# Kernel tuning notes

Measured on AMD Instinct MI355X. Metric: run time of the kernel, lower is better.

## Reference

```python
import jax, jax.numpy as jnp
import numpy as np

SHIFTS = [1, 2, 4]  # matches init_kwargs 'shifts' (all in range 0 < s < channels)


def setup_inputs() -> dict:
    key = jax.random.key(0)
    k1, k2, k3 = jax.random.split(key, 3)
    B, H, L, D = 4, 1, 2048, 512
    factor = 4
    proj_in = 2 * len(SHIFTS) * D  # cli_mode='full' -> 2 components per shift
    x = jax.random.normal(k1, (B, H, L, D), dtype=jnp.float32)
    W = jax.random.normal(k2, (factor, D), dtype=jnp.float32) * 0.05
    # glorot-ish scale for the projection kernel
    proj_kernel = jax.random.normal(k3, (proj_in, D), dtype=jnp.float32) * (1.0 / np.sqrt(proj_in))
    proj_bias = jnp.zeros((D,), dtype=jnp.float32)
    return {"x": x, "W": W, "proj_kernel": proj_kernel, "proj_bias": proj_bias}


def reference(x, W, proj_kernel, proj_bias):
    # x: (B, H, L, D); W: (k, D) slot multivectors
    k, D = W.shape
    B, H, L, _ = x.shape
    # coarse[-1] treated as zeros; non-anchor slots source previous coarse vector
    coarse_prev = jnp.pad(x, ((0, 0), (0, 0), (1, 0), (0, 0)))[:, :, :-1, :]
    # src: (B, H, L, k, D) — slots 0..k-2 from coarse_prev, slot k-1 (anchor) from x
    src = jnp.concatenate(
        [jnp.repeat(coarse_prev[:, :, :, None, :], k - 1, axis=3),
         x[:, :, :, None, :]],
        axis=3,
    )
    W_b = W[None, None, None, :, :]  # (1,1,1,k,D)
    components = []
    for s in SHIFTS:
        src_s = jnp.roll(src, s, axis=-1)
        W_s_b = jnp.roll(W, s, axis=-1)[None, None, None, :, :]
        sw = src * W_s_b
        components.append(sw - W_b * src_s)        # wedge part
        components.append(jax.nn.silu(sw))          # inner part (full mode)
    g = jnp.concatenate(components, axis=-1)  # (B,H,L,k, 2*len(shifts)*D)
    fine = jnp.einsum('bhlkc,cd->bhlkd', g, proj_kernel) + proj_bias
    return fine.reshape(B, H, L * k, D)
```

## Files before the change

kernel.cpp:

```cpp
#include <hip/hip_runtime.h>
#include <cstdint>
#include <cstddef>

#define D_DIM 512
#define L_DIM 2048
#define KB_DIM 2048
#define KS_DIM 1536
#define NROWS_X 2049
#define M_TOT 32768

typedef __bf16 bf16x8 __attribute__((ext_vector_type(8)));
typedef float  f32x4  __attribute__((ext_vector_type(4)));

__device__ __forceinline__ unsigned f2bf(float f) {
  unsigned u = __float_as_uint(f);
  u += 0x7FFF + ((u >> 16) & 1);
  return u >> 16;
}
__device__ __forceinline__ float bf2f(unsigned short u) {
  return __uint_as_float(((unsigned)u) << 16);
}
__device__ __forceinline__ void gld_lds16(const void* g, void* l) {
  __builtin_amdgcn_global_load_lds((const __attribute__((address_space(1))) void*)g,
                                   (__attribute__((address_space(3))) void*)l,
                                   16, 0, 0);
}

__global__ __launch_bounds__(256) void prep(
    const float* __restrict__ x, const float* __restrict__ W, const float* __restrict__ P,
    unsigned short* __restrict__ XbfZ, unsigned short* __restrict__ Ball,
    unsigned short* __restrict__ GS, int doGS) {
  __shared__ unsigned short WtabL[6144];
  const int tid = threadIdx.x;

  if (blockIdx.x < 2048) {
    for (int i = tid; i < 6144; i += 256) {
      const int c = i & 511; const int rest = i >> 9;
      const int si = rest % 3; const int jj = rest / 3;
      WtabL[i] = (unsigned short)f2bf(W[jj * 512 + ((c - (1 << si)) & 511)]);
    }
    __syncthreads();

    const int r = tid >> 6, lane = tid & 63;
    const int gr = blockIdx.x * 4 + r;
    const int b = gr >> 11, l = gr & 2047;

    const float4* xr = reinterpret_cast<const float4*>(x) + ((size_t)(b * L_DIM + l)) * 128 + lane * 2;
    const float4 v0 = xr[0], v1 = xr[1];
    union U { uint4 q; unsigned short s[8]; };
    U va;
    va.q.x = f2bf(v0.x) | (f2bf(v0.y) << 16);
    va.q.y = f2bf(v0.z) | (f2bf(v0.w) << 16);
    va.q.z = f2bf(v1.x) | (f2bf(v1.y) << 16);
    va.q.w = f2bf(v1.z) | (f2bf(v1.w) << 16);
    *reinterpret_cast<uint4*>(XbfZ + ((size_t)(b * NROWS_X + l + 1)) * 512 + lane * 8) = va.q;

    if (doGS) {
      #pragma unroll
      for (int j = 0; j < 4; ++j) {
        const int lam = (j < 3) ? (l + 1) : l;
        const bool wr = (j == 3) || (l < 2047);
        unsigned short* o = GS + ((size_t)((j * 4 + b) * L_DIM + lam)) * KS_DIM + lane * 8;
        #pragma unroll
        for (int si = 0; si < 3; ++si) {
          U wa;
          wa.q = *reinterpret_cast<const uint4*>(&WtabL[(j * 3 + si) * 512 + lane * 8]);
          unsigned res[4];
          #pragma unroll
          for (int e = 0; e < 4; ++e) {
            float s0 = bf2f(va.s[2 * e])     * bf2f(wa.s[2 * e]);
            float s1 = bf2f(va.s[2 * e + 1]) * bf2f(wa.s[2 * e + 1]);
            float g0 = s0 * __builtin_amdgcn_rcpf(1.f + __expf(-s0));
            float g1 = s1 * __builtin_amdgcn_rcpf(1.f + __expf(-s1));
            res[e] = f2bf(g0) | (f2bf(g1) << 16);
          }
          if (wr) {
            uint4 ov = {res[0], res[1], res[2], res[3]};
            *reinterpret_cast<uint4*>(o + si * 512) = ov;
          }
        }
      }
    }
    if (l == 2047) {
      const uint4 z = {0u, 0u, 0u, 0u};
      *reinterpret_cast<uint4*>(XbfZ + ((size_t)(b * NROWS_X)) * 512 + lane * 8) = z;
      if (doGS) {
        #pragma unroll
        for (int j = 0; j < 3; ++j)
          #pragma unroll
          for (int si = 0; si < 3; ++si)
            *reinterpret_cast<uint4*>(GS + ((size_t)((j * 4 + b) * L_DIM)) * KS_DIM + si * 512 + lane * 8) = z;
      }
    }
    return;
  }

  const int bx = blockIdx.x - 2048;
  const int j = bx >> 6, dt = (bx >> 3) & 7, ct = bx & 7;
  const int d = dt * 64 + (tid & 63);
  const int cbase = ct * 64 + (tid >> 6) * 16;
  unsigned short bufd[16];
  unsigned short bufs[3][16];
  #pragma unroll
  for (int cc = 0; cc < 16; ++cc) {
    const int c = cbase + cc;
    float qd = 0.f;
    #pragma unroll
    for (int si = 0; si < 3; ++si) {
      const int s = 1 << si;
      const int cm = (c - s) & 511, cp = (c + s) & 511;
      qd += W[j * 512 + cm] * P[((size_t)(2 * si) * 512 + c) * 512 + d]
          - W[j * 512 + cp] * P[((size_t)(2 * si) * 512 + cp) * 512 + d];
      bufs[si][cc] = (unsigned short)f2bf(P[((size_t)(2 * si + 1) * 512 + c) * 512 + d]);
    }
    bufd[cc] = (unsigned short)f2bf(qd);
  }
  unsigned short* row = Ball + (size_t)(j * 512 + d) * KB_DIM;
  *reinterpret_cast<uint4*>(&row[cbase])     = *reinterpret_cast<uint4*>(&bufd[0]);
  *reinterpret_cast<uint4*>(&row[cbase + 8]) = *reinterpret_cast<uint4*>(&bufd[8]);
  #pragma unroll
  for (int si = 0; si < 3; ++si) {
    *reinterpret_cast<uint4*>(&row[512 + si * 512 + cbase])     = *reinterpret_cast<uint4*>(&bufs[si][0]);
    *reinterpret_cast<uint4*>(&row[512 + si * 512 + cbase + 8]) = *reinterpret_cast<uint4*>(&bufs[si][8]);
  }
}

#define BARR asm volatile("s_barrier" ::: "memory")
#define VMW(N) asm volatile("s_waitcnt vmcnt(" #N ")" ::: "memory")

#define READ_A(MH, BUF) do { \
  _Pragma("unroll") \
  for (int mf = 0; mf < 4; ++mf) { \
    a[mf][0] = __builtin_bit_cast(bf16x8, *reinterpret_cast<const uint4*>(&A_lds[BUF][aRow[mf] + (MH)*4096 + p0])); \
    a[mf][1] = __builtin_bit_cast(bf16x8, *reinterpret_cast<const uint4*>(&A_lds[BUF][aRow[mf] + (MH)*4096 + p1])); \
  } } while (0)

#define READ_B(NH, BUF, BB) do { \
  _Pragma("unroll") \
  for (int nf = 0; nf < 2; ++nf) { \
    BB[nf][0] = __builtin_bit_cast(bf16x8, *reinterpret_cast<const uint4*>(&B_lds[BUF][bRow[nf] + (NH)*2048 + p0])); \
    BB[nf][1] = __builtin_bit_cast(bf16x8, *reinterpret_cast<const uint4*>(&B_lds[BUF][bRow[nf] + (NH)*2048 + p1])); \
  } } while (0)

#define MFMA_Q(MH, NH, BB) do { \
  _Pragma("unroll") \
  for (int mf = 0; mf < 4; ++mf) { \
    _Pragma("unroll") \
    for (int nf = 0; nf < 2; ++nf) { \
      acc[(MH)*4+mf][(NH)*2+nf] = __builtin_amdgcn_mfma_f32_16x16x32_bf16(a[mf][0], BB[nf][0], acc[(MH)*4+mf][(NH)*2+nf], 0, 0, 0); \
      acc[(MH)*4+mf][(NH)*2+nf] = __builtin_amdgcn_mfma_f32_16x16x32_bf16(a[mf][1], BB[nf][1], acc[(MH)*4+mf][(NH)*2+nf], 0, 0, 0); \
    } } } while (0)

__global__ __launch_bounds__(512, 2) void gemm8(
    const unsigned short* __restrict__ XbfZ, const unsigned short* __restrict__ GS,
    const unsigned short* __restrict__ Ball, const float* __restrict__ bias,
    float* __restrict__ out) {
  __shared__ alignas(16) unsigned short A_lds[2][16384];
  __shared__ alignas(16) unsigned short B_lds[2][16384];

  const int tid = threadIdx.x;
  const int bid = blockIdx.x;
  const int wid = (bid & 7) * 32 + (bid >> 3);
  const int mtile = wid >> 1;
  const int ntile = wid & 1;
  const int j  = mtile >> 5;
  const int b  = (mtile >> 3) & 3;
  const int l0 = (mtile & 7) * 256;
  const int n0 = ntile * 256;
  const size_t mbase = (size_t)((j * 4 + b) * L_DIM + l0);

  const int srow = tid >> 3;
  const int c8   = (tid & 7) ^ (srow & 7);
  const unsigned short* pXd = XbfZ + ((size_t)(b * NROWS_X + (j == 3) + l0 + srow)) * 512 + c8 * 8;
  const unsigned short* pGS = GS + (mbase + srow) * (size_t)KS_DIM + c8 * 8;
  const unsigned short* pB  = Ball + ((size_t)(j * 512 + n0 + srow)) * KB_DIM + c8 * 8;
  const int ldsSlot = tid * 8;

  auto stageA = [&](int TT, int h, int bufi) {
    unsigned short* dst = &A_lds[bufi][h * 8192 + ldsSlot];
    if (TT < 8) {
      const unsigned short* s = pXd + (size_t)h * 128 * 512 + TT * 64;
      gld_lds16(s, dst);
      gld_lds16(s + 64 * 512, dst + 4096);
    } else {
      const unsigned short* s = pGS + (size_t)h * 128 * KS_DIM + (TT - 8) * 64;
      gld_lds16(s, dst);
      gld_lds16(s + 64 * KS_DIM, dst + 4096);
    }
  };
  auto stageB = [&](int TT, int h, int bufi) {
    const unsigned short* s = pB + (size_t)h * 128 * KB_DIM + TT * 64;
    unsigned short* dst = &B_lds[bufi][h * 8192 + ldsSlot];
    gld_lds16(s, dst);
    gld_lds16(s + 64 * KB_DIM, dst + 4096);
  };

  const int lane = tid & 63, wv = tid >> 6;
  const int wm = wv >> 2, wn = wv & 3;
  const int l16 = lane & 15, quad = lane >> 4;
  const int p0 = ((quad)     ^ (l16 & 7)) * 8;
  const int p1 = ((quad + 4) ^ (l16 & 7)) * 8;
  int aRow[4], bRow[2];
  #pragma unroll
  for (int mf = 0; mf < 4; ++mf) aRow[mf] = (wm * 128 + mf * 16 + l16) * 64;
  #pragma unroll
  for (int nf = 0; nf < 2; ++nf) bRow[nf] = (wn * 64 + nf * 16 + l16) * 64;

  f32x4 acc[8][4];
  #pragma unroll
  for (int i = 0; i < 8; ++i)
    #pragma unroll
    for (int n = 0; n < 4; ++n)
      acc[i][n] = f32x4{0.f, 0.f, 0.f, 0.f};

  bf16x8 a[4][2], b0[2][2], b1[2][2];

  stageB(0, 0, 0); stageB(0, 1, 0);
  stageA(0, 0, 0); stageA(0, 1, 0);
  stageB(1, 0, 1); stageB(1, 1, 1);
  VMW(4);
  BARR;

  for (int T = 0; T < 32; ++T) {
    const int cur = T & 1, nxt = cur ^ 1;
    if (T + 1 < 32) { stageA(T + 1, 0, nxt); stageA(T + 1, 1, nxt); }
    READ_A(0, cur);
    READ_B(0, cur, b0);
    READ_B(1, cur, b1);
    __builtin_amdgcn_s_setprio(1);
    MFMA_Q(0, 0, b0);
    MFMA_Q(0, 1, b1);
    __builtin_amdgcn_s_setprio(0);
    BARR;
    if (T + 2 < 32) { stageB(T + 2, 0, cur); stageB(T + 2, 1, cur); }
    READ_A(1, cur);
    __builtin_amdgcn_s_setprio(1);
    MFMA_Q(1, 1, b1);
    MFMA_Q(1, 0, b0);
    __builtin_amdgcn_s_setprio(0);
    if (T < 30) {
      VMW(4);
      BARR;
    } else if (T == 30) {
      VMW(0);
      BARR;
    }
  }

  #pragma unroll
  for (int nfg = 0; nfg < 4; ++nfg) {
    const int d = n0 + wn * 64 + nfg * 16 + l16;
    const float bv = bias[d];
    #pragma unroll
    for (int mfg = 0; mfg < 8; ++mfg) {
      const int lrow = l0 + wm * 128 + mfg * 16 + quad * 4;
      #pragma unroll
      for (int rg = 0; rg < 4; ++rg) {
        out[((size_t)(b * L_DIM + lrow + rg) * 4 + j) * D_DIM + d] = acc[mfg][nfg][rg] + bv;
      }
    }
  }
}

__global__ __launch_bounds__(256, 2) void fused_gemm(
    const unsigned short* __restrict__ XbfZ, const unsigned short* __restrict__ Ball,
    const float* __restrict__ W, const float* __restrict__ bias,
    float* __restrict__ out) {
  __shared__ alignas(16) unsigned short Vt[2][4096];
  __shared__ alignas(16) unsigned short Bt[2][8192];
  __shared__ alignas(16) unsigned short At[128 * 40];
  __shared__ alignas(16) unsigned short Wr[3 * 512];

  const int tid = threadIdx.x;
  const int nt = blockIdx.x & 1;
  const int mt = blockIdx.x >> 1;
  const int j  = mt >> 6;
  const int b  = (mt >> 4) & 3;
  const int lt = mt & 15;
  const int l0 = lt * 128;
  const int n0 = nt * 256;
  const int base_l = l0 - ((j == 3) ? 0 : 1);

  #pragma unroll
  for (int i = 0; i < 6; ++i) {
    const int idx = tid + i * 256;
    const int si = idx >> 9, c = idx & 511, s = 1 << si;
    Wr[idx] = (unsigned short)f2bf(W[j * 512 + ((c - s) & 511)]);
  }

  const int lane = tid & 63, wv = tid >> 6;
  const int qv = (lane & 3) ^ ((lane >> 4) & 3);
  const int rsub = lane >> 2;
  const unsigned short* gA0 = XbfZ + ((size_t)(b * NROWS_X + 1 + base_l + (wv * 2) * 16 + rsub)) * 512 + qv * 8;
  const unsigned short* gA1 = gA0 + (size_t)16 * 512;
  const unsigned short* gB[4];
  #pragma unroll
  for (int pi = 0; pi < 4; ++pi)
    gB[pi] = Ball + (size_t)(j * 512 + n0 + (wv * 4 + pi) * 16 + rsub) * KB_DIM + qv * 8;
  const int vOff0 = wv * 1024 + lane * 8;
  const int bOff0 = wv * 2048 + lane * 8;

  const int am = tid >> 1;
  const int akh = (tid & 1) * 16;
  const int ch0 = (tid & 1) * 2;
  const int sswz = (am >> 2) & 3;
  unsigned short* aDst = &At[am * 40 + akh];

  const int l16 = lane & 15, quad = lane >> 4;
  const int wm = wv >> 1, wn = wv & 1;
  const int fsw = (l16 >> 2) & 3;
  const int aVoff = (wm * 64 + l16) * 32 + ((quad ^ fsw)) * 8;
  const int aSoff = (wm * 64 + l16) * 40 + quad * 8;
  const int bOffF = (wn * 128 + l16) * 32 + ((quad ^ fsw)) * 8;

  f32x4 acc[4][8];
  #pragma unroll
  for (int i = 0; i < 4; ++i)
    #pragma unroll
    for (int n = 0; n < 8; ++n)
      acc[i][n] = f32x4{0.f, 0.f, 0.f, 0.f};

  {
    gld_lds16(gA0, &Vt[0][vOff0]);
    gld_lds16(gA1, &Vt[0][vOff0 + 512]);
    #pragma unroll
    for (int pi = 0; pi < 4; ++pi)
      gld_lds16(gB[pi], &Bt[0][bOff0 + pi * 512]);
  }

  for (int it = 0; it < 64; ++it) {
    const int buf = it & 1;
    const int kk0 = it * 32;
    const int gi = kk0 >> 9;

    __syncthreads();

    if (it + 1 < 64) {
      const int nk = kk0 + 32;
      const int nv = nk & 511;
      gld_lds16(gA0 + nv, &Vt[buf ^ 1][vOff0]);
      gld_lds16(gA1 + nv, &Vt[buf ^ 1][vOff0 + 512]);
      #pragma unroll
      for (int pi = 0; pi < 4; ++pi)
        gld_lds16(gB[pi] + nk, &Bt[buf ^ 1][bOff0 + pi * 512]);
    }

    bf16x8 af[4], bfr[8];
    if (gi == 0) {
      #pragma unroll
      for (int mi = 0; mi < 4; ++mi) {
        uint4 r = *reinterpret_cast<const uint4*>(&Vt[buf][aVoff + mi * 512]);
        af[mi] = __builtin_bit_cast(bf16x8, r);
      }
    } else {
      const int si = gi - 1;
      const int ccbase = (kk0 & 511) + akh;
      uint4 v0 = *reinterpret_cast<const uint4*>(&Vt[buf][(am * 4 + ((ch0)     ^ sswz)) * 8]);
      uint4 v1 = *reinterpret_cast<const uint4*>(&Vt[buf][(am * 4 + ((ch0 + 1) ^ sswz)) * 8]);
      uint4 w0 = *reinterpret_cast<const uint4*>(&Wr[si * 512 + ccbase]);
      uint4 w1 = *reinterpret_cast<const uint4*>(&Wr[si * 512 + ccbase + 8]);
      union U { uint4 q[2]; unsigned short s[16]; };
      U va, wa; va.q[0] = v0; va.q[1] = v1; wa.q[0] = w0; wa.q[1] = w1;
      unsigned res[8];
      #pragma unroll
      for (int e = 0; e < 8; ++e) {
        float s0 = bf2f(va.s[2 * e])     * bf2f(wa.s[2 * e]);
        float s1 = bf2f(va.s[2 * e + 1]) * bf2f(wa.s[2 * e + 1]);
        float g0 = s0 * __builtin_amdgcn_rcpf(1.f + __expf(-s0));
        float g1 = s1 * __builtin_amdgcn_rcpf(1.f + __expf(-s1));
        res[e] = f2bf(g0) | (f2bf(g1) << 16);
      }
      uint4 o0 = {res[0], res[1], res[2], res[3]};
      uint4 o1 = {res[4], res[5], res[6], res[7]};
      *reinterpret_cast<uint4*>(aDst) = o0;
      *reinterpret_cast<uint4*>(aDst + 8) = o1;
      __syncthreads();
      #pragma unroll
      for (int mi = 0; mi < 4; ++mi) {
        uint4 r = *reinterpret_cast<const uint4*>(&At[aSoff + mi * 640]);
        af[mi] = __builtin_bit_cast(bf16x8, r);
      }
    }
    #pragma unroll
    for (int ni = 0; ni < 8; ++ni) {
      uint4 r = *reinterpret_cast<const uint4*>(&Bt[buf][bOffF + ni * 512]);
      bfr[ni] = __builtin_bit_cast(bf16x8, r);
    }
    #pragma unroll
    for (int mi = 0; mi < 4; ++mi)
      #pragma unroll
      for (int ni = 0; ni < 8; ++ni)
        acc[mi][ni] = __builtin_amdgcn_mfma_f32_16x16x32_bf16(af[mi], bfr[ni], acc[mi][ni], 0, 0, 0);
  }

  #pragma unroll
  for (int ni = 0; ni < 8; ++ni) {
    const int d = n0 + wn * 128 + ni * 16 + l16;
    const float bv = bias[d];
    #pragma unroll
    for (int mi = 0; mi < 4; ++mi) {
      const int lrow = l0 + wm * 64 + mi * 16 + quad * 4;
      #pragma unroll
      for (int rg = 0; rg < 4; ++rg) {
        out[((size_t)(b * L_DIM + lrow + rg) * 4 + j) * D_DIM + d] = acc[mi][ni][rg] + bv;
      }
    }
  }
}

extern "C" void kernel_launch(void* const* d_in, const int* in_sizes, int n_in,
                              void* d_out, int out_size, void* d_ws, size_t ws_size,
                              hipStream_t stream) {
  const float* x    = (const float*)d_in[0];
  const float* W    = (const float*)d_in[1];
  const float* P    = (const float*)d_in[2];
  const float* bias = (const float*)d_in[3];
  float* out = (float*)d_out;

  unsigned short* XbfZ = (unsigned short*)d_ws;
  unsigned short* Ball = XbfZ + (size_t)4 * NROWS_X * 512;
  unsigned short* GS   = Ball + (size_t)4 * 512 * KB_DIM + 6144;
  const size_t need_bytes =
      ((size_t)4 * NROWS_X * 512 + (size_t)4 * 512 * KB_DIM + 6144 +
       (size_t)M_TOT * KS_DIM) * 2;
  const bool primary = ws_size >= need_bytes;

  prep<<<2304, 256, 0, stream>>>(x, W, P, XbfZ, Ball, GS, primary ? 1 : 0);
  if (primary) {
    gemm8<<<dim3(256), dim3(512), 0, stream>>>(XbfZ, GS, Ball, bias, out);
  } else {
    fused_gemm<<<512, 256, 0, stream>>>(XbfZ, Ball, W, bias, out);
  }
}
```

Measured before the change: 175.5 us.

## Compute SiLU operand on the fly inside GEMM instead of materializing GS buffer

The prep kernel no longer writes the large bf16 SiLU operand buffer (GS, about 100MB); it only converts x to bf16 and builds the folded weight matrix. The GEMM now computes the SiLU(x*W_shift) A-tiles itself. For each k-tile it reads the x row from global into registers, applies the product and SiLU after the first MFMA half, and writes the result into the swizzled LDS buffer. K-tiles are interleaved so each x chunk is reused across the three shifts. This removes a large write and re-read of global memory, at the cost of extra VALU work and register loads inside the GEMM pipeline, plus added lgkmcnt waits.

Result: slower. 189.2 us (+7.8%).

```diff
diff --git a/kernel.cpp b/kernel.cpp
--- a/kernel.cpp
+++ b/kernel.cpp
@@ -5,9 +5,7 @@
 #define D_DIM 512
 #define L_DIM 2048
 #define KB_DIM 2048
-#define KS_DIM 1536
 #define NROWS_X 2049
-#define M_TOT 32768
 
 typedef __bf16 bf16x8 __attribute__((ext_vector_type(8)));
 typedef float  f32x4  __attribute__((ext_vector_type(4)));
@@ -28,74 +26,27 @@
 
 __global__ __launch_bounds__(256) void prep(
     const float* __restrict__ x, const float* __restrict__ W, const float* __restrict__ P,
-    unsigned short* __restrict__ XbfZ, unsigned short* __restrict__ Ball,
-    unsigned short* __restrict__ GS, int doGS) {
-  __shared__ unsigned short WtabL[6144];
+    unsigned short* __restrict__ XbfZ, unsigned short* __restrict__ Ball) {
   const int tid = threadIdx.x;
-
-  if (blockIdx.x < 2048) {
-    for (int i = tid; i < 6144; i += 256) {
-      const int c = i & 511; const int rest = i >> 9;
-      const int si = rest % 3; const int jj = rest / 3;
-      WtabL[i] = (unsigned short)f2bf(W[jj * 512 + ((c - (1 << si)) & 511)]);
-    }
-    __syncthreads();
-
-    const int r = tid >> 6, lane = tid & 63;
-    const int gr = blockIdx.x * 4 + r;
-    const int b = gr >> 11, l = gr & 2047;
-
-    const float4* xr = reinterpret_cast<const float4*>(x) + ((size_t)(b * L_DIM + l)) * 128 + lane * 2;
-    const float4 v0 = xr[0], v1 = xr[1];
-    union U { uint4 q; unsigned short s[8]; };
-    U va;
-    va.q.x = f2bf(v0.x) | (f2bf(v0.y) << 16);
-    va.q.y = f2bf(v0.z) | (f2bf(v0.w) << 16);
-    va.q.z = f2bf(v1.x) | (f2bf(v1.y) << 16);
-    va.q.w = f2bf(v1.z) | (f2bf(v1.w) << 16);
-    *reinterpret_cast<uint4*>(XbfZ + ((size_t)(b * NROWS_X + l + 1)) * 512 + lane * 8) = va.q;
-
-    if (doGS) {
-      #pragma unroll
-      for (int j = 0; j < 4; ++j) {
-        const int lam = (j < 3) ? (l + 1) : l;
-        const bool wr = (j == 3) || (l < 2047);
-        unsigned short* o = GS + ((size_t)((j * 4 + b) * L_DIM + lam)) * KS_DIM + lane * 8;
-        #pragma unroll
-        for (int si = 0; si < 3; ++si) {
-          U wa;
-          wa.q = *reinterpret_cast<const uint4*>(&WtabL[(j * 3 + si) * 512 + lane * 8]);
-          unsigned res[4];
-          #pragma unroll
-          for (int e = 0; e < 4; ++e) {
-            float s0 = bf2f(va.s[2 * e])     * bf2f(wa.s[2 * e]);
-            float s1 = bf2f(va.s[2 * e + 1]) * bf2f(wa.s[2 * e + 1]);
-            float g0 = s0 * __builtin_amdgcn_rcpf(1.f + __expf(-s0));
-            float g1 = s1 * __builtin_amdgcn_rcpf(1.f + __expf(-s1));
-            res[e] = f2bf(g0) | (f2bf(g1) << 16);
-          }
-          if (wr) {
-            uint4 ov = {res[0], res[1], res[2], res[3]};
-            *reinterpret_cast<uint4*>(o + si * 512) = ov;
-          }
-        }
-      }
-    }
-    if (l == 2047) {
-      const uint4 z = {0u, 0u, 0u, 0u};
-      *reinterpret_cast<uint4*>(XbfZ + ((size_t)(b * NROWS_X)) * 512 + lane * 8) = z;
-      if (doGS) {
-        #pragma unroll
-        for (int j = 0; j < 3; ++j)
-          #pragma unroll
-          for (int si = 0; si < 3; ++si)
-            *reinterpret_cast<uint4*>(GS + ((size_t)((j * 4 + b) * L_DIM)) * KS_DIM + si * 512 + lane * 8) = z;
-      }
-    }
+  if (blockIdx.x >= 256) {
+    const int u = (blockIdx.x - 256) * 256 + tid;
+    const int b = u / (NROWS_X * 64);
+    const int rr = (u >> 6) % NROWS_X;
+    const int c8 = u & 63;
+    uint4 p = {0u, 0u, 0u, 0u};
+    if (rr > 0) {
+      const float4* src = reinterpret_cast<const float4*>(x) +
+                          ((size_t)(b * L_DIM + rr - 1)) * 128 + c8 * 2;
+      const float4 v0 = src[0], v1 = src[1];
+      p.x = f2bf(v0.x) | (f2bf(v0.y) << 16);
+      p.y = f2bf(v0.z) | (f2bf(v0.w) << 16);
+      p.z = f2bf(v1.x) | (f2bf(v1.y) << 16);
+      p.w = f2bf(v1.z) | (f2bf(v1.w) << 16);
+    }
+    reinterpret_cast<uint4*>(XbfZ)[((size_t)(b * NROWS_X + rr)) * 64 + c8] = p;
     return;
   }
-
-  const int bx = blockIdx.x - 2048;
+  const int bx = blockIdx.x;
   const int j = bx >> 6, dt = (bx >> 3) & 7, ct = bx & 7;
   const int d = dt * 64 + (tid & 63);
   const int cbase = ct * 64 + (tid >> 6) * 16;
@@ -127,6 +78,8 @@
 
 #define BARR asm volatile("s_barrier" ::: "memory")
 #define VMW(N) asm volatile("s_waitcnt vmcnt(" #N ")" ::: "memory")
+#define LGKM0 asm volatile("s_waitcnt lgkmcnt(0)" ::: "memory")
+#define KT(S) (((((S) & 3)) << 3) + ((S) >> 2))
 
 #define READ_A(MH, BUF) do { \
   _Pragma("unroll") \
@@ -151,12 +104,13 @@
       acc[(MH)*4+mf][(NH)*2+nf] = __builtin_amdgcn_mfma_f32_16x16x32_bf16(a[mf][1], BB[nf][1], acc[(MH)*4+mf][(NH)*2+nf], 0, 0, 0); \
     } } } while (0)
 
-__global__ __launch_bounds__(512, 2) void gemm8(
-    const unsigned short* __restrict__ XbfZ, const unsigned short* __restrict__ GS,
-    const unsigned short* __restrict__ Ball, const float* __restrict__ bias,
+__global__ __launch_bounds__(512, 2) void gemmcs(
+    const unsigned short* __restrict__ XbfZ, const unsigned short* __restrict__ Ball,
+    const float* __restrict__ W, const float* __restrict__ bias,
     float* __restrict__ out) {
   __shared__ alignas(16) unsigned short A_lds[2][16384];
   __shared__ alignas(16) unsigned short B_lds[2][16384];
+  __shared__ alignas(16) unsigned short Wt[1536];
 
   const int tid = threadIdx.x;
   const int bid = blockIdx.x;
@@ -167,33 +121,40 @@
   const int b  = (mtile >> 3) & 3;
   const int l0 = (mtile & 7) * 256;
   const int n0 = ntile * 256;
-  const size_t mbase = (size_t)((j * 4 + b) * L_DIM + l0);
+
+  for (int i = tid; i < 1536; i += 512) {
+    const int si = i >> 9, c = i & 511;
+    Wt[i] = (unsigned short)f2bf(W[j * 512 + ((c - (1 << si)) & 511)]);
+  }
 
   const int srow = tid >> 3;
   const int c8   = (tid & 7) ^ (srow & 7);
   const unsigned short* pXd = XbfZ + ((size_t)(b * NROWS_X + (j == 3) + l0 + srow)) * 512 + c8 * 8;
-  const unsigned short* pGS = GS + (mbase + srow) * (size_t)KS_DIM + c8 * 8;
   const unsigned short* pB  = Ball + ((size_t)(j * 512 + n0 + srow)) * KB_DIM + c8 * 8;
   const int ldsSlot = tid * 8;
 
-  auto stageA = [&](int TT, int h, int bufi) {
-    unsigned short* dst = &A_lds[bufi][h * 8192 + ldsSlot];
-    if (TT < 8) {
-      const unsigned short* s = pXd + (size_t)h * 128 * 512 + TT * 64;
+  auto stageXd = [&](int cb, int bufi) {
+    #pragma unroll
+    for (int h = 0; h < 2; ++h) {
+      const unsigned short* s = pXd + (size_t)h * 128 * 512 + cb * 64;
+      unsigned short* dst = &A_lds[bufi][h * 8192 + ldsSlot];
       gld_lds16(s, dst);
       gld_lds16(s + 64 * 512, dst + 4096);
-    } else {
-      const unsigned short* s = pGS + (size_t)h * 128 * KS_DIM + (TT - 8) * 64;
+    }
+  };
+  auto stageB = [&](int kt, int bufi) {
+    #pragma unroll
+    for (int h = 0; h < 2; ++h) {
+      const unsigned short* s = pB + (size_t)h * 128 * KB_DIM + kt * 64;
+      unsigned short* dst = &B_lds[bufi][h * 8192 + ldsSlot];
       gld_lds16(s, dst);
-      gld_lds16(s + 64 * KS_DIM, dst + 4096);
+      gld_lds16(s + 64 * KB_DIM, dst + 4096);
     }
   };
-  auto stageB = [&](int TT, int h, int bufi) {
-    const unsigned short* s = pB + (size_t)h * 128 * KB_DIM + TT * 64;
-    unsigned short* dst = &B_lds[bufi][h * 8192 + ldsSlot];
-    gld_lds16(s, dst);
-    gld_lds16(s + 64 * KB_DIM, dst + 4096);
-  };
+
+  const int prow = tid >> 1;
+  const int phalf = tid & 1;
+  const unsigned short* pXr = XbfZ + ((size_t)(b * NROWS_X + (j == 3) + l0 + prow)) * 512 + phalf * 32;
 
   const int lane = tid & 63, wv = tid >> 6;
   const int wm = wv >> 2, wn = wv & 3;
@@ -215,15 +176,27 @@
 
   bf16x8 a[4][2], b0[2][2], b1[2][2];
 
-  stageB(0, 0, 0); stageB(0, 1, 0);
-  stageA(0, 0, 0); stageA(0, 1, 0);
-  stageB(1, 0, 1); stageB(1, 1, 1);
+  stageXd(0, 0);
+  stageB(KT(0), 0);
+  stageB(KT(1), 1);
+  LGKM0;
   VMW(4);
   BARR;
 
-  for (int T = 0; T < 32; ++T) {
-    const int cur = T & 1, nxt = cur ^ 1;
-    if (T + 1 < 32) { stageA(T + 1, 0, nxt); stageA(T + 1, 1, nxt); }
+  for (int s = 0; s < 32; ++s) {
+    const int cur = s & 1, nxt = cur ^ 1;
+    const int f1 = (s + 1) & 3;
+    const int cb1 = (s + 1) >> 2;
+    uint4 xv[4];
+    if (s < 31) {
+      if (f1 == 0) {
+        stageXd(cb1, nxt);
+      } else {
+        #pragma unroll
+        for (int k = 0; k < 4; ++k)
+          xv[k] = *reinterpret_cast<const uint4*>(pXr + cb1 * 64 + k * 8);
+      }
+    }
     READ_A(0, cur);
     READ_B(0, cur, b0);
     READ_B(1, cur, b1);
@@ -232,16 +205,42 @@
     MFMA_Q(0, 1, b1);
     __builtin_amdgcn_s_setprio(0);
     BARR;
-    if (T + 2 < 32) { stageB(T + 2, 0, cur); stageB(T + 2, 1, cur); }
+    if (s < 31 && f1 != 0) {
+      VMW(0);
+      const int si = f1 - 1;
+      const int wtbase = si * 512 + cb1 * 64 + phalf * 32;
+      #pragma unroll
+      for (int k = 0; k < 4; ++k) {
+        union UU { uint4 q; unsigned short sh[8]; } vv, ww;
+        vv.q = xv[k];
+        ww.q = *reinterpret_cast<const uint4*>(&Wt[wtbase + k * 8]);
+        unsigned res[4];
+        #pragma unroll
+        for (int e = 0; e < 4; ++e) {
+          float s0 = bf2f(vv.sh[2 * e])     * bf2f(ww.sh[2 * e]);
+          float s1 = bf2f(vv.sh[2 * e + 1]) * bf2f(ww.sh[2 * e + 1]);
+          float g0 = s0 * __builtin_amdgcn_rcpf(1.f + __expf(-s0));
+          float g1 = s1 * __builtin_amdgcn_rcpf(1.f + __expf(-s1));
+          res[e] = f2bf(g0) | (f2bf(g1) << 16);
+        }
+        const int lc = phalf * 4 + k;
+        const int pos = lc ^ (prow & 7);
+        uint4 ov = {res[0], res[1], res[2], res[3]};
+        *reinterpret_cast<uint4*>(&A_lds[nxt][prow * 64 + pos * 8]) = ov;
+      }
+    }
+    if (s + 2 < 32) stageB(KT(s + 2), cur);
     READ_A(1, cur);
     __builtin_amdgcn_s_setprio(1);
     MFMA_Q(1, 1, b1);
     MFMA_Q(1, 0, b0);
     __builtin_amdgcn_s_setprio(0);
-    if (T < 30) {
+    if (s < 30) {
+      LGKM0;
       VMW(4);
       BARR;
-    } else if (T == 30) {
+    } else if (s == 30) {
+      LGKM0;
       VMW(0);
       BARR;
     }
@@ -257,152 +256,6 @@
       #pragma unroll
       for (int rg = 0; rg < 4; ++rg) {
         out[((size_t)(b * L_DIM + lrow + rg) * 4 + j) * D_DIM + d] = acc[mfg][nfg][rg] + bv;
-      }
-    }
-  }
-}
-
-__global__ __launch_bounds__(256, 2) void fused_gemm(
-    const unsigned short* __restrict__ XbfZ, const unsigned short* __restrict__ Ball,
-    const float* __restrict__ W, const float* __restrict__ bias,
-    float* __restrict__ out) {
-  __shared__ alignas(16) unsigned short Vt[2][4096];
-  __shared__ alignas(16) unsigned short Bt[2][8192];
-  __shared__ alignas(16) unsigned short At[128 * 40];
-  __shared__ alignas(16) unsigned short Wr[3 * 512];
-
-  const int tid = threadIdx.x;
-  const int nt = blockIdx.x & 1;
-  const int mt = blockIdx.x >> 1;
-  const int j  = mt >> 6;
-  const int b  = (mt >> 4) & 3;
-  const int lt = mt & 15;
-  const int l0 = lt * 128;
-  const int n0 = nt * 256;
-  const int base_l = l0 - ((j == 3) ? 0 : 1);
-
-  #pragma unroll
-  for (int i = 0; i < 6; ++i) {
-    const int idx = tid + i * 256;
-    const int si = idx >> 9, c = idx & 511, s = 1 << si;
-    Wr[idx] = (unsigned short)f2bf(W[j * 512 + ((c - s) & 511)]);
-  }
-
-  const int lane = tid & 63, wv = tid >> 6;
-  const int qv = (lane & 3) ^ ((lane >> 4) & 3);
-  const int rsub = lane >> 2;
-  const unsigned short* gA0 = XbfZ + ((size_t)(b * NROWS_X + 1 + base_l + (wv * 2) * 16 + rsub)) * 512 + qv * 8;
-  const unsigned short* gA1 = gA0 + (size_t)16 * 512;
-  const unsigned short* gB[4];
-  #pragma unroll
-  for (int pi = 0; pi < 4; ++pi)
-    gB[pi] = Ball + (size_t)(j * 512 + n0 + (wv * 4 + pi) * 16 + rsub) * KB_DIM + qv * 8;
-  const int vOff0 = wv * 1024 + lane * 8;
-  const int bOff0 = wv * 2048 + lane * 8;
-
-  const int am = tid >> 1;
-  const int akh = (tid & 1) * 16;
-  const int ch0 = (tid & 1) * 2;
-  const int sswz = (am >> 2) & 3;
-  unsigned short* aDst = &At[am * 40 + akh];
-
-  const int l16 = lane & 15, quad = lane >> 4;
-  const int wm = wv >> 1, wn = wv & 1;
-  const int fsw = (l16 >> 2) & 3;
-  const int aVoff = (wm * 64 + l16) * 32 + ((quad ^ fsw)) * 8;
-  const int aSoff = (wm * 64 + l16) * 40 + quad * 8;
-  const int bOffF = (wn * 128 + l16) * 32 + ((quad ^ fsw)) * 8;
-
-  f32x4 acc[4][8];
-  #pragma unroll
-  for (int i = 0; i < 4; ++i)
-    #pragma unroll
-    for (int n = 0; n < 8; ++n)
-      acc[i][n] = f32x4{0.f, 0.f, 0.f, 0.f};
-
-  {
-    gld_lds16(gA0, &Vt[0][vOff0]);
-    gld_lds16(gA1, &Vt[0][vOff0 + 512]);
-    #pragma unroll
-    for (int pi = 0; pi < 4; ++pi)
-      gld_lds16(gB[pi], &Bt[0][bOff0 + pi * 512]);
-  }
-
-  for (int it = 0; it < 64; ++it) {
-    const int buf = it & 1;
-    const int kk0 = it * 32;
-    const int gi = kk0 >> 9;
-
-    __syncthreads();
-
-    if (it + 1 < 64) {
-      const int nk = kk0 + 32;
-      const int nv = nk & 511;
-      gld_lds16(gA0 + nv, &Vt[buf ^ 1][vOff0]);
-      gld_lds16(gA1 + nv, &Vt[buf ^ 1][vOff0 + 512]);
-      #pragma unroll
-      for (int pi = 0; pi < 4; ++pi)
-        gld_lds16(gB[pi] + nk, &Bt[buf ^ 1][bOff0 + pi * 512]);
-    }
-
-    bf16x8 af[4], bfr[8];
-    if (gi == 0) {
-      #pragma unroll
-      for (int mi = 0; mi < 4; ++mi) {
-        uint4 r = *reinterpret_cast<const uint4*>(&Vt[buf][aVoff + mi * 512]);
-        af[mi] = __builtin_bit_cast(bf16x8, r);
-      }
-    } else {
-      const int si = gi - 1;
-      const int ccbase = (kk0 & 511) + akh;
-      uint4 v0 = *reinterpret_cast<const uint4*>(&Vt[buf][(am * 4 + ((ch0)     ^ sswz)) * 8]);
-      uint4 v1 = *reinterpret_cast<const uint4*>(&Vt[buf][(am * 4 + ((ch0 + 1) ^ sswz)) * 8]);
-      uint4 w0 = *reinterpret_cast<const uint4*>(&Wr[si * 512 + ccbase]);
-      uint4 w1 = *reinterpret_cast<const uint4*>(&Wr[si * 512 + ccbase + 8]);
-      union U { uint4 q[2]; unsigned short s[16]; };
-      U va, wa; va.q[0] = v0; va.q[1] = v1; wa.q[0] = w0; wa.q[1] = w1;
-      unsigned res[8];
-      #pragma unroll
-      for (int e = 0; e < 8; ++e) {
-        float s0 = bf2f(va.s[2 * e])     * bf2f(wa.s[2 * e]);
-        float s1 = bf2f(va.s[2 * e + 1]) * bf2f(wa.s[2 * e + 1]);
-        float g0 = s0 * __builtin_amdgcn_rcpf(1.f + __expf(-s0));
-        float g1 = s1 * __builtin_amdgcn_rcpf(1.f + __expf(-s1));
-        res[e] = f2bf(g0) | (f2bf(g1) << 16);
-      }
-      uint4 o0 = {res[0], res[1], res[2], res[3]};
-      uint4 o1 = {res[4], res[5], res[6], res[7]};
-      *reinterpret_cast<uint4*>(aDst) = o0;
-      *reinterpret_cast<uint4*>(aDst + 8) = o1;
-      __syncthreads();
-      #pragma unroll
-      for (int mi = 0; mi < 4; ++mi) {
-        uint4 r = *reinterpret_cast<const uint4*>(&At[aSoff + mi * 640]);
-        af[mi] = __builtin_bit_cast(bf16x8, r);
-      }
-    }
-    #pragma unroll
-    for (int ni = 0; ni < 8; ++ni) {
-      uint4 r = *reinterpret_cast<const uint4*>(&Bt[buf][bOffF + ni * 512]);
-      bfr[ni] = __builtin_bit_cast(bf16x8, r);
-    }
-    #pragma unroll
-    for (int mi = 0; mi < 4; ++mi)
-      #pragma unroll
-      for (int ni = 0; ni < 8; ++ni)
-        acc[mi][ni] = __builtin_amdgcn_mfma_f32_16x16x32_bf16(af[mi], bfr[ni], acc[mi][ni], 0, 0, 0);
-  }
-
-  #pragma unroll
-  for (int ni = 0; ni < 8; ++ni) {
-    const int d = n0 + wn * 128 + ni * 16 + l16;
-    const float bv = bias[d];
-    #pragma unroll
-    for (int mi = 0; mi < 4; ++mi) {
-      const int lrow = l0 + wm * 64 + mi * 16 + quad * 4;
-      #pragma unroll
-      for (int rg = 0; rg < 4; ++rg) {
-        out[((size_t)(b * L_DIM + lrow + rg) * 4 + j) * D_DIM + d] = acc[mi][ni][rg] + bv;
       }
     }
   }
@@ -419,16 +272,7 @@
 
   unsigned short* XbfZ = (unsigned short*)d_ws;
   unsigned short* Ball = XbfZ + (size_t)4 * NROWS_X * 512;
-  unsigned short* GS   = Ball + (size_t)4 * 512 * KB_DIM + 6144;
-  const size_t need_bytes =
-      ((size_t)4 * NROWS_X * 512 + (size_t)4 * 512 * KB_DIM + 6144 +
-       (size_t)M_TOT * KS_DIM) * 2;
-  const bool primary = ws_size >= need_bytes;
-
-  prep<<<2304, 256, 0, stream>>>(x, W, P, XbfZ, Ball, GS, primary ? 1 : 0);
-  if (primary) {
-    gemm8<<<dim3(256), dim3(512), 0, stream>>>(XbfZ, GS, Ball, bias, out);
-  } else {
-    fused_gemm<<<512, 256, 0, stream>>>(XbfZ, Ball, W, bias, out);
-  }
-}
+
+  prep<<<2305, 256, 0, stream>>>(x, W, P, XbfZ, Ball);
+  gemmcs<<<dim3(256), dim3(512), 0, stream>>>(XbfZ, Ball, W, bias, out);
+}
```

## Triple-buffer A tiles in LDS and reorder MFMA issue per k-chunk

Applied to the files above, without the earlier changes.

The A operand moves from double to triple buffering in LDS. Each A tile is now prefetched two k-steps ahead, matching B, and the wait count is raised so two stages stay in flight. The MFMA loop is reordered to walk k-chunks outermost and reuse each A fragment across all four N fragments. This is meant to hide more global-to-LDS latency behind the matrix work. In exchange it grows LDS per block to 160KB, which fills the CU's LDS and rules out a second resident block.

Result: no change. 175.8 us (+0.2%).

```diff
diff --git a/kernel.cpp b/kernel.cpp
--- a/kernel.cpp
+++ b/kernel.cpp
@@ -128,34 +128,36 @@
 #define BARR asm volatile("s_barrier" ::: "memory")
 #define VMW(N) asm volatile("s_waitcnt vmcnt(" #N ")" ::: "memory")
 
-#define READ_A(MH, BUF) do { \
+#define READ_A(MH, AP) do { \
   _Pragma("unroll") \
   for (int mf = 0; mf < 4; ++mf) { \
-    a[mf][0] = __builtin_bit_cast(bf16x8, *reinterpret_cast<const uint4*>(&A_lds[BUF][aRow[mf] + (MH)*4096 + p0])); \
-    a[mf][1] = __builtin_bit_cast(bf16x8, *reinterpret_cast<const uint4*>(&A_lds[BUF][aRow[mf] + (MH)*4096 + p1])); \
+    a[mf][0] = __builtin_bit_cast(bf16x8, *reinterpret_cast<const uint4*>(&(AP)[aRow[mf] + (MH)*4096 + p0])); \
+    a[mf][1] = __builtin_bit_cast(bf16x8, *reinterpret_cast<const uint4*>(&(AP)[aRow[mf] + (MH)*4096 + p1])); \
   } } while (0)
 
-#define READ_B(NH, BUF, BB) do { \
+#define READ_B(NH, BP, BB) do { \
   _Pragma("unroll") \
   for (int nf = 0; nf < 2; ++nf) { \
-    BB[nf][0] = __builtin_bit_cast(bf16x8, *reinterpret_cast<const uint4*>(&B_lds[BUF][bRow[nf] + (NH)*2048 + p0])); \
-    BB[nf][1] = __builtin_bit_cast(bf16x8, *reinterpret_cast<const uint4*>(&B_lds[BUF][bRow[nf] + (NH)*2048 + p1])); \
+    BB[nf][0] = __builtin_bit_cast(bf16x8, *reinterpret_cast<const uint4*>(&(BP)[bRow[nf] + (NH)*2048 + p0])); \
+    BB[nf][1] = __builtin_bit_cast(bf16x8, *reinterpret_cast<const uint4*>(&(BP)[bRow[nf] + (NH)*2048 + p1])); \
   } } while (0)
 
-#define MFMA_Q(MH, NH, BB) do { \
+#define MFMA_ROW(MH) do { \
   _Pragma("unroll") \
-  for (int mf = 0; mf < 4; ++mf) { \
+  for (int kc = 0; kc < 2; ++kc) { \
     _Pragma("unroll") \
-    for (int nf = 0; nf < 2; ++nf) { \
-      acc[(MH)*4+mf][(NH)*2+nf] = __builtin_amdgcn_mfma_f32_16x16x32_bf16(a[mf][0], BB[nf][0], acc[(MH)*4+mf][(NH)*2+nf], 0, 0, 0); \
-      acc[(MH)*4+mf][(NH)*2+nf] = __builtin_amdgcn_mfma_f32_16x16x32_bf16(a[mf][1], BB[nf][1], acc[(MH)*4+mf][(NH)*2+nf], 0, 0, 0); \
+    for (int mf = 0; mf < 4; ++mf) { \
+      acc[(MH)*4+mf][0] = __builtin_amdgcn_mfma_f32_16x16x32_bf16(a[mf][kc], b0[0][kc], acc[(MH)*4+mf][0], 0, 0, 0); \
+      acc[(MH)*4+mf][1] = __builtin_amdgcn_mfma_f32_16x16x32_bf16(a[mf][kc], b0[1][kc], acc[(MH)*4+mf][1], 0, 0, 0); \
+      acc[(MH)*4+mf][2] = __builtin_amdgcn_mfma_f32_16x16x32_bf16(a[mf][kc], b1[0][kc], acc[(MH)*4+mf][2], 0, 0, 0); \
+      acc[(MH)*4+mf][3] = __builtin_amdgcn_mfma_f32_16x16x32_bf16(a[mf][kc], b1[1][kc], acc[(MH)*4+mf][3], 0, 0, 0); \
     } } } while (0)
 
 __global__ __launch_bounds__(512, 2) void gemm8(
     const unsigned short* __restrict__ XbfZ, const unsigned short* __restrict__ GS,
     const unsigned short* __restrict__ Ball, const float* __restrict__ bias,
     float* __restrict__ out) {
-  __shared__ alignas(16) unsigned short A_lds[2][16384];
+  __shared__ alignas(16) unsigned short A_lds[3][16384];
   __shared__ alignas(16) unsigned short B_lds[2][16384];
 
   const int tid = threadIdx.x;
@@ -176,23 +178,29 @@
   const unsigned short* pB  = Ball + ((size_t)(j * 512 + n0 + srow)) * KB_DIM + c8 * 8;
   const int ldsSlot = tid * 8;
 
-  auto stageA = [&](int TT, int h, int bufi) {
-    unsigned short* dst = &A_lds[bufi][h * 8192 + ldsSlot];
-    if (TT < 8) {
-      const unsigned short* s = pXd + (size_t)h * 128 * 512 + TT * 64;
+  auto stageA = [&](int TT, int bufi) {
+    #pragma unroll
+    for (int h = 0; h < 2; ++h) {
+      unsigned short* dst = &A_lds[bufi][h * 8192 + ldsSlot];
+      if (TT < 8) {
+        const unsigned short* s = pXd + (size_t)h * 128 * 512 + TT * 64;
+        gld_lds16(s, dst);
+        gld_lds16(s + 64 * 512, dst + 4096);
+      } else {
+        const unsigned short* s = pGS + (size_t)h * 128 * KS_DIM + (TT - 8) * 64;
+        gld_lds16(s, dst);
+        gld_lds16(s + 64 * KS_DIM, dst + 4096);
+      }
+    }
+  };
+  auto stageB = [&](int TT, int bufi) {
+    #pragma unroll
+    for (int h = 0; h < 2; ++h) {
+      const unsigned short* s = pB + (size_t)h * 128 * KB_DIM + TT * 64;
+      unsigned short* dst = &B_lds[bufi][h * 8192 + ldsSlot];
       gld_lds16(s, dst);
-      gld_lds16(s + 64 * 512, dst + 4096);
-    } else {
-      const unsigned short* s = pGS + (size_t)h * 128 * KS_DIM + (TT - 8) * 64;
-      gld_lds16(s, dst);
-      gld_lds16(s + 64 * KS_DIM, dst + 4096);
-    }
-  };
-  auto stageB = [&](int TT, int h, int bufi) {
-    const unsigned short* s = pB + (size_t)h * 128 * KB_DIM + TT * 64;
-    unsigned short* dst = &B_lds[bufi][h * 8192 + ldsSlot];
-    gld_lds16(s, dst);
-    gld_lds16(s + 64 * KB_DIM, dst + 4096);
+      gld_lds16(s + 64 * KB_DIM, dst + 4096);
+    }
   };
 
   const int lane = tid & 63, wv = tid >> 6;
@@ -215,36 +223,40 @@
 
   bf16x8 a[4][2], b0[2][2], b1[2][2];
 
-  stageB(0, 0, 0); stageB(0, 1, 0);
-  stageA(0, 0, 0); stageA(0, 1, 0);
-  stageB(1, 0, 1); stageB(1, 1, 1);
-  VMW(4);
+  stageA(0, 0);
+  stageB(0, 0);
+  stageA(1, 1);
+  stageB(1, 1);
+  VMW(8);
   BARR;
 
+  int ra = 0;
   for (int T = 0; T < 32; ++T) {
-    const int cur = T & 1, nxt = cur ^ 1;
-    if (T + 1 < 32) { stageA(T + 1, 0, nxt); stageA(T + 1, 1, nxt); }
-    READ_A(0, cur);
-    READ_B(0, cur, b0);
-    READ_B(1, cur, b1);
+    const int cur = T & 1;
+    const int rs = (ra >= 1) ? (ra - 1) : 2;
+    const unsigned short* Ac = A_lds[ra];
+    const unsigned short* Bc = B_lds[cur];
+    if (T + 2 < 32) stageA(T + 2, rs);
+    READ_A(0, Ac);
+    READ_B(0, Bc, b0);
+    READ_B(1, Bc, b1);
     __builtin_amdgcn_s_setprio(1);
-    MFMA_Q(0, 0, b0);
-    MFMA_Q(0, 1, b1);
+    MFMA_ROW(0);
     __builtin_amdgcn_s_setprio(0);
     BARR;
-    if (T + 2 < 32) { stageB(T + 2, 0, cur); stageB(T + 2, 1, cur); }
-    READ_A(1, cur);
+    if (T + 2 < 32) stageB(T + 2, cur);
+    READ_A(1, Ac);
     __builtin_amdgcn_s_setprio(1);
-    MFMA_Q(1, 1, b1);
-    MFMA_Q(1, 0, b0);
+    MFMA_ROW(1);
     __builtin_amdgcn_s_setprio(0);
     if (T < 30) {
-      VMW(4);
+      VMW(8);
       BARR;
     } else if (T == 30) {
       VMW(0);
       BARR;
     }
+    ra = (ra >= 2) ? 0 : (ra + 1);
   }
 
   #pragma unroll
```

## Replace 256x256 GEMM tiles with 128x128 tiles and a triple-buffered K pipeline

Applied to the files above, without the earlier changes.

The primary GEMM moves from 256 blocks of 512 threads on 256x256 tiles (K step 64, double buffered) to 1024 blocks of 256 threads on 128x128 tiles (K step 32, three LDS stages, prefetch distance 2). The LDS swizzle and fragment offsets are rebuilt for the 32-wide rows. The aim is more blocks per CU and better latency hiding on a 256-CU part. The cost is less operand reuse per tile, more global and LDS traffic, and twice as many barriers along K.

Result: slower. 206.7 us (+17.7%).

```diff
diff --git a/kernel.cpp b/kernel.cpp
--- a/kernel.cpp
+++ b/kernel.cpp
@@ -128,135 +128,114 @@
 #define BARR asm volatile("s_barrier" ::: "memory")
 #define VMW(N) asm volatile("s_waitcnt vmcnt(" #N ")" ::: "memory")
 
-#define READ_A(MH, BUF) do { \
-  _Pragma("unroll") \
-  for (int mf = 0; mf < 4; ++mf) { \
-    a[mf][0] = __builtin_bit_cast(bf16x8, *reinterpret_cast<const uint4*>(&A_lds[BUF][aRow[mf] + (MH)*4096 + p0])); \
-    a[mf][1] = __builtin_bit_cast(bf16x8, *reinterpret_cast<const uint4*>(&A_lds[BUF][aRow[mf] + (MH)*4096 + p1])); \
-  } } while (0)
-
-#define READ_B(NH, BUF, BB) do { \
-  _Pragma("unroll") \
-  for (int nf = 0; nf < 2; ++nf) { \
-    BB[nf][0] = __builtin_bit_cast(bf16x8, *reinterpret_cast<const uint4*>(&B_lds[BUF][bRow[nf] + (NH)*2048 + p0])); \
-    BB[nf][1] = __builtin_bit_cast(bf16x8, *reinterpret_cast<const uint4*>(&B_lds[BUF][bRow[nf] + (NH)*2048 + p1])); \
-  } } while (0)
-
-#define MFMA_Q(MH, NH, BB) do { \
-  _Pragma("unroll") \
-  for (int mf = 0; mf < 4; ++mf) { \
-    _Pragma("unroll") \
-    for (int nf = 0; nf < 2; ++nf) { \
-      acc[(MH)*4+mf][(NH)*2+nf] = __builtin_amdgcn_mfma_f32_16x16x32_bf16(a[mf][0], BB[nf][0], acc[(MH)*4+mf][(NH)*2+nf], 0, 0, 0); \
-      acc[(MH)*4+mf][(NH)*2+nf] = __builtin_amdgcn_mfma_f32_16x16x32_bf16(a[mf][1], BB[nf][1], acc[(MH)*4+mf][(NH)*2+nf], 0, 0, 0); \
-    } } } while (0)
-
-__global__ __launch_bounds__(512, 2) void gemm8(
+__global__ __launch_bounds__(256, 3) void gemm128(
     const unsigned short* __restrict__ XbfZ, const unsigned short* __restrict__ GS,
     const unsigned short* __restrict__ Ball, const float* __restrict__ bias,
     float* __restrict__ out) {
-  __shared__ alignas(16) unsigned short A_lds[2][16384];
-  __shared__ alignas(16) unsigned short B_lds[2][16384];
+  __shared__ alignas(16) unsigned short A_lds[3][4096];
+  __shared__ alignas(16) unsigned short B_lds[3][4096];
 
   const int tid = threadIdx.x;
   const int bid = blockIdx.x;
-  const int wid = (bid & 7) * 32 + (bid >> 3);
-  const int mtile = wid >> 1;
-  const int ntile = wid & 1;
-  const int j  = mtile >> 5;
-  const int b  = (mtile >> 3) & 3;
-  const int l0 = (mtile & 7) * 256;
-  const int n0 = ntile * 256;
+  const int wid = (bid & 7) * 128 + (bid >> 3);
+  const int mtile = wid >> 2;
+  const int ntile = wid & 3;
+  const int j  = mtile >> 6;
+  const int b  = (mtile >> 4) & 3;
+  const int l0 = (mtile & 15) * 128;
+  const int n0 = ntile * 128;
   const size_t mbase = (size_t)((j * 4 + b) * L_DIM + l0);
 
-  const int srow = tid >> 3;
-  const int c8   = (tid & 7) ^ (srow & 7);
-  const unsigned short* pXd = XbfZ + ((size_t)(b * NROWS_X + (j == 3) + l0 + srow)) * 512 + c8 * 8;
-  const unsigned short* pGS = GS + (mbase + srow) * (size_t)KS_DIM + c8 * 8;
-  const unsigned short* pB  = Ball + ((size_t)(j * 512 + n0 + srow)) * KB_DIM + c8 * 8;
+  const int srow = tid >> 2;
+  const int spos = tid & 3;
+  const int sc   = spos ^ (srow & 3) ^ ((srow >> 2) & 3);
+  const unsigned short* pXd = XbfZ + ((size_t)(b * NROWS_X + (j == 3) + l0 + srow)) * 512 + sc * 8;
+  const unsigned short* pGS = GS + (mbase + srow) * (size_t)KS_DIM + sc * 8;
+  const unsigned short* pB  = Ball + ((size_t)(j * 512 + n0 + srow)) * KB_DIM + sc * 8;
   const int ldsSlot = tid * 8;
 
-  auto stageA = [&](int TT, int h, int bufi) {
-    unsigned short* dst = &A_lds[bufi][h * 8192 + ldsSlot];
-    if (TT < 8) {
-      const unsigned short* s = pXd + (size_t)h * 128 * 512 + TT * 64;
+  auto stageA = [&](int TT, int bufi) {
+    unsigned short* dst = &A_lds[bufi][ldsSlot];
+    if (TT < 16) {
+      const unsigned short* s = pXd + TT * 32;
       gld_lds16(s, dst);
-      gld_lds16(s + 64 * 512, dst + 4096);
+      gld_lds16(s + 64 * 512, dst + 2048);
     } else {
-      const unsigned short* s = pGS + (size_t)h * 128 * KS_DIM + (TT - 8) * 64;
+      const unsigned short* s = pGS + (TT - 16) * 32;
       gld_lds16(s, dst);
-      gld_lds16(s + 64 * KS_DIM, dst + 4096);
+      gld_lds16(s + 64 * KS_DIM, dst + 2048);
     }
   };
-  auto stageB = [&](int TT, int h, int bufi) {
-    const unsigned short* s = pB + (size_t)h * 128 * KB_DIM + TT * 64;
-    unsigned short* dst = &B_lds[bufi][h * 8192 + ldsSlot];
+  auto stageB = [&](int TT, int bufi) {
+    const unsigned short* s = pB + TT * 32;
+    unsigned short* dst = &B_lds[bufi][ldsSlot];
     gld_lds16(s, dst);
-    gld_lds16(s + 64 * KB_DIM, dst + 4096);
+    gld_lds16(s + 64 * KB_DIM, dst + 2048);
   };
 
   const int lane = tid & 63, wv = tid >> 6;
-  const int wm = wv >> 2, wn = wv & 3;
+  const int wm = wv >> 1, wn = wv & 1;
   const int l16 = lane & 15, quad = lane >> 4;
-  const int p0 = ((quad)     ^ (l16 & 7)) * 8;
-  const int p1 = ((quad + 4) ^ (l16 & 7)) * 8;
-  int aRow[4], bRow[2];
-  #pragma unroll
-  for (int mf = 0; mf < 4; ++mf) aRow[mf] = (wm * 128 + mf * 16 + l16) * 64;
-  #pragma unroll
-  for (int nf = 0; nf < 2; ++nf) bRow[nf] = (wn * 64 + nf * 16 + l16) * 64;
-
-  f32x4 acc[8][4];
-  #pragma unroll
-  for (int i = 0; i < 8; ++i)
+  const int rp = (quad ^ (l16 & 3) ^ ((l16 >> 2) & 3)) * 8;
+  int aOff[4], bOff[4];
+  #pragma unroll
+  for (int mf = 0; mf < 4; ++mf) aOff[mf] = (wm * 64 + mf * 16 + l16) * 32 + rp;
+  #pragma unroll
+  for (int nf = 0; nf < 4; ++nf) bOff[nf] = (wn * 64 + nf * 16 + l16) * 32 + rp;
+
+  f32x4 acc[4][4];
+  #pragma unroll
+  for (int i = 0; i < 4; ++i)
     #pragma unroll
     for (int n = 0; n < 4; ++n)
       acc[i][n] = f32x4{0.f, 0.f, 0.f, 0.f};
 
-  bf16x8 a[4][2], b0[2][2], b1[2][2];
-
-  stageB(0, 0, 0); stageB(0, 1, 0);
-  stageA(0, 0, 0); stageA(0, 1, 0);
-  stageB(1, 0, 1); stageB(1, 1, 1);
+  bf16x8 a[4], bf[4];
+
+  stageA(0, 0); stageB(0, 0);
+  stageA(1, 1); stageB(1, 1);
   VMW(4);
   BARR;
 
-  for (int T = 0; T < 32; ++T) {
-    const int cur = T & 1, nxt = cur ^ 1;
-    if (T + 1 < 32) { stageA(T + 1, 0, nxt); stageA(T + 1, 1, nxt); }
-    READ_A(0, cur);
-    READ_B(0, cur, b0);
-    READ_B(1, cur, b1);
+  int cur = 0;
+  for (int T = 0; T < 64; ++T) {
+    const int rs = (cur >= 1) ? (cur - 1) : 2;
+    if (T + 2 < 64) { stageA(T + 2, rs); stageB(T + 2, rs); }
+    const unsigned short* Ac = A_lds[cur];
+    const unsigned short* Bc = B_lds[cur];
+    #pragma unroll
+    for (int mf = 0; mf < 4; ++mf)
+      a[mf] = __builtin_bit_cast(bf16x8, *reinterpret_cast<const uint4*>(&Ac[aOff[mf]]));
+    #pragma unroll
+    for (int nf = 0; nf < 4; ++nf)
+      bf[nf] = __builtin_bit_cast(bf16x8, *reinterpret_cast<const uint4*>(&Bc[bOff[nf]]));
     __builtin_amdgcn_s_setprio(1);
-    MFMA_Q(0, 0, b0);
-    MFMA_Q(0, 1, b1);
+    #pragma unroll
+    for (int mf = 0; mf < 4; ++mf)
+      #pragma unroll
+      for (int nf = 0; nf < 4; ++nf)
+        acc[mf][nf] = __builtin_amdgcn_mfma_f32_16x16x32_bf16(a[mf], bf[nf], acc[mf][nf], 0, 0, 0);
     __builtin_amdgcn_s_setprio(0);
-    BARR;
-    if (T + 2 < 32) { stageB(T + 2, 0, cur); stageB(T + 2, 1, cur); }
-    READ_A(1, cur);
-    __builtin_amdgcn_s_setprio(1);
-    MFMA_Q(1, 1, b1);
-    MFMA_Q(1, 0, b0);
-    __builtin_amdgcn_s_setprio(0);
-    if (T < 30) {
+    if (T < 62) {
       VMW(4);
       BARR;
-    } else if (T == 30) {
+    } else if (T == 62) {
       VMW(0);
       BARR;
     }
-  }
-
-  #pragma unroll
-  for (int nfg = 0; nfg < 4; ++nfg) {
-    const int d = n0 + wn * 64 + nfg * 16 + l16;
+    cur = (cur >= 2) ? 0 : (cur + 1);
+  }
+
+  #pragma unroll
+  for (int nf = 0; nf < 4; ++nf) {
+    const int d = n0 + wn * 64 + nf * 16 + l16;
     const float bv = bias[d];
     #pragma unroll
-    for (int mfg = 0; mfg < 8; ++mfg) {
-      const int lrow = l0 + wm * 128 + mfg * 16 + quad * 4;
+    for (int mf = 0; mf < 4; ++mf) {
+      const int lrow = l0 + wm * 64 + mf * 16 + quad * 4;
       #pragma unroll
       for (int rg = 0; rg < 4; ++rg) {
-        out[((size_t)(b * L_DIM + lrow + rg) * 4 + j) * D_DIM + d] = acc[mfg][nfg][rg] + bv;
+        out[((size_t)(b * L_DIM + lrow + rg) * 4 + j) * D_DIM + d] = acc[mf][nf][rg] + bv;
       }
     }
   }
@@ -427,7 +406,7 @@
 
   prep<<<2304, 256, 0, stream>>>(x, W, P, XbfZ, Ball, GS, primary ? 1 : 0);
   if (primary) {
-    gemm8<<<dim3(256), dim3(512), 0, stream>>>(XbfZ, GS, Ball, bias, out);
+    gemm128<<<dim3(1024), dim3(256), 0, stream>>>(XbfZ, GS, Ball, bias, out);
   } else {
     fused_gemm<<<512, 256, 0, stream>>>(XbfZ, Ball, W, bias, out);
   }
```
